# Performance work log

Hardware: AMD Instinct MI355X
Metric: run time of the kernel (lower is better)

## Reference

```python
import jax, jax.numpy as jnp
import numpy as np

N_NODES = 100000
N_EDGES = 1000000
D = 128           # operand size = 4 segments of u=32
N_SEG = 4


def setup_inputs() -> dict:
    key = jax.random.key(0)
    k1, k2, k3, k4, k5 = jax.random.split(key, 5)
    x = jax.random.normal(k1, (N_NODES, D), dtype=jnp.float32)   # node features (input 0)
    y = jax.random.normal(k2, (N_EDGES, D), dtype=jnp.float32)   # per-edge features (input 1)
    coeffs = jax.random.normal(k3, (N_SEG,), dtype=jnp.float32)  # stacked path coefficients, one per path (seg_i, seg_i, seg_i)
    src = jax.random.randint(k4, (N_EDGES,), 0, N_NODES, dtype=jnp.int64)  # input_indices[0]
    dst = jax.random.randint(k5, (N_EDGES,), 0, N_NODES, dtype=jnp.int64)  # output_indices[0]
    return {"x": x, "y": y, "coeffs": coeffs, "src": src, "dst": dst, "n_nodes": N_NODES}


def reference(x, y, coeffs, src, dst, n_nodes):
    # Segmented TP, subscripts 'u_u_u': per path p=(i,i,i), out_seg_i = c_i * x_seg_i * y_seg_i.
    # Broadcast per-segment path coefficient across its u=32 lanes.
    seg_size = x.shape[-1] // coeffs.shape[0]
    c = jnp.repeat(coeffs, seg_size)                 # [D]
    # gather (input_indices) -> fused elementwise TP -> scatter-add (output_indices)
    prod = x[src] * y * c                            # [E, D]
    out = jax.ops.segment_sum(prod, dst, num_segments=n_nodes)  # [N, D]
    return out
```

## Files before the change

### kernel.cpp

```cpp
#include <hip/hip_runtime.h>

#define N_EDGES  1000000
#define N_NODES  100000
#define DIM      128

#define WS_COUNTS   0
#define WS_COUNTS2  100000
#define WS_OFFSETS  200000
#define WS_BLKSUMS  300000
#define WS_BLKOFFS  300128
#define WS_SORTED   300256

#define SCAN_CHUNK  1024
#define NBLK        ((N_NODES + SCAN_CHUNK - 1) / SCAN_CHUNK)

__global__ void __launch_bounds__(256)
hist_kernel(const int* __restrict__ dst, unsigned* __restrict__ counts)
{
    int e = blockIdx.x * 256 + threadIdx.x;
    if (e < N_EDGES) atomicAdd(&counts[dst[e]], 1u);
}

__global__ void __launch_bounds__(256)
reduce_blocks(const unsigned* __restrict__ counts, unsigned* __restrict__ blkSums)
{
    __shared__ unsigned lds[256];
    int b = blockIdx.x, t = threadIdx.x;
    int base = b * SCAN_CHUNK + t * 4;
    unsigned s = 0;
    #pragma unroll
    for (int k = 0; k < 4; k++) { int i = base + k; if (i < N_NODES) s += counts[i]; }
    lds[t] = s; __syncthreads();
    for (int off = 128; off > 0; off >>= 1) {
        if (t < off) lds[t] += lds[t + off];
        __syncthreads();
    }
    if (t == 0) blkSums[b] = lds[0];
}

__global__ void scan_sums(const unsigned* __restrict__ blkSums, unsigned* __restrict__ blkOffs)
{
    if (threadIdx.x == 0) {
        unsigned r = 0;
        for (int i = 0; i < NBLK; i++) { blkOffs[i] = r; r += blkSums[i]; }
    }
}

__global__ void __launch_bounds__(256)
scan_blocks(const unsigned* __restrict__ counts, const unsigned* __restrict__ blkOffs,
            unsigned* __restrict__ offsets)
{
    __shared__ unsigned lds[256];
    int b = blockIdx.x, t = threadIdx.x;
    int base = b * SCAN_CHUNK + t * 4;
    unsigned v[4]; unsigned s = 0;
    #pragma unroll
    for (int k = 0; k < 4; k++) { int i = base + k; v[k] = (i < N_NODES) ? counts[i] : 0u; s += v[k]; }
    lds[t] = s; __syncthreads();
    for (int off = 1; off < 256; off <<= 1) {
        unsigned add = (t >= off) ? lds[t - off] : 0u;
        __syncthreads();
        lds[t] += add;
        __syncthreads();
    }
    unsigned excl = (t == 0) ? 0u : lds[t - 1];
    unsigned run = blkOffs[b] + excl;
    #pragma unroll
    for (int k = 0; k < 4; k++) { int i = base + k; if (i < N_NODES) offsets[i] = run; run += v[k]; }
}

__global__ void __launch_bounds__(256)
scatter_kernel(const int* __restrict__ dst, const unsigned* __restrict__ offsets,
               unsigned* __restrict__ cursors, unsigned* __restrict__ sorted)
{
    int e = blockIdx.x * 256 + threadIdx.x;
    if (e >= N_EDGES) return;
    int d = dst[e];
    unsigned pos = offsets[d] + atomicAdd(&cursors[d], 1u);
    sorted[pos] = (unsigned)e;
}

__global__ void __launch_bounds__(256)
gather_reduce(const float* __restrict__ x, const float* __restrict__ y,
              const float* __restrict__ coeffs, const int* __restrict__ src,
              const unsigned* __restrict__ offsets, const unsigned* __restrict__ counts,
              const unsigned* __restrict__ sorted, float* __restrict__ out)
{
    int wave = threadIdx.x >> 6;
    int lane = threadIdx.x & 63;
    int n = blockIdx.x * 4 + wave;
    if (n >= N_NODES) return;

    const int col = lane * 2;
    float c = coeffs[lane >> 4];
    unsigned start = offsets[n];
    unsigned cnt   = counts[n];
    unsigned j = start, end = start + cnt;

    float ax = 0.f, ay = 0.f;
    for (; j + 2 <= end; j += 2) {
        unsigned e0 = sorted[j], e1 = sorted[j + 1];
        int s0 = src[e0], s1 = src[e1];
        float2 y0 = *reinterpret_cast<const float2*>(y + (size_t)e0 * DIM + col);
        float2 x0 = *reinterpret_cast<const float2*>(x + (size_t)s0 * DIM + col);
        float2 y1 = *reinterpret_cast<const float2*>(y + (size_t)e1 * DIM + col);
        float2 x1 = *reinterpret_cast<const float2*>(x + (size_t)s1 * DIM + col);
        ax += x0.x * y0.x; ay += x0.y * y0.y;
        ax += x1.x * y1.x; ay += x1.y * y1.y;
    }
    if (j < end) {
        unsigned e0 = sorted[j];
        int s0 = src[e0];
        float2 y0 = *reinterpret_cast<const float2*>(y + (size_t)e0 * DIM + col);
        float2 x0 = *reinterpret_cast<const float2*>(x + (size_t)s0 * DIM + col);
        ax += x0.x * y0.x; ay += x0.y * y0.y;
    }
    float2 r; r.x = c * ax; r.y = c * ay;
    *reinterpret_cast<float2*>(out + (size_t)n * DIM + col) = r;
}

extern "C" void kernel_launch(void* const* d_in, const int* in_sizes, int n_in,
                              void* d_out, int out_size, void* d_ws, size_t ws_size,
                              hipStream_t stream)
{
    const float* x      = (const float*)d_in[0];
    const float* y      = (const float*)d_in[1];
    const float* coeffs = (const float*)d_in[2];
    const int*   src    = (const int*)d_in[3];
    const int*   dst    = (const int*)d_in[4];
    float* out = (float*)d_out;

    unsigned* ws = (unsigned*)d_ws;
    unsigned* counts  = ws + WS_COUNTS;
    unsigned* cursors = ws + WS_COUNTS2;
    unsigned* offsets = ws + WS_OFFSETS;
    unsigned* blkSums = ws + WS_BLKSUMS;
    unsigned* blkOffs = ws + WS_BLKOFFS;
    unsigned* sorted  = ws + WS_SORTED;

    hipMemsetAsync(d_ws, 0, 200000 * sizeof(unsigned), stream);

    hist_kernel<<<(N_EDGES + 255) / 256, 256, 0, stream>>>(dst, counts);
    reduce_blocks<<<NBLK, 256, 0, stream>>>(counts, blkSums);
    scan_sums<<<1, 64, 0, stream>>>(blkSums, blkOffs);
    scan_blocks<<<NBLK, 256, 0, stream>>>(counts, blkOffs, offsets);
    scatter_kernel<<<(N_EDGES + 255) / 256, 256, 0, stream>>>(dst, offsets, cursors, sorted);
    gather_reduce<<<(N_NODES + 3) / 4, 256, 0, stream>>>(x, y, coeffs, src, offsets, counts, sorted, out);
}
```

Before: 867.1 us.

## Replace prefix scan with atomic bucket allocation and pack src into sorted pairs

Replaces the three-kernel prefix scan with one kernel that gives each wave a contiguous bucket range through an atomic counter. Buckets are no longer globally ordered, but each node's range stays contiguous. The scatter now stores (edge, src) pairs, so the gather no longer does a dependent lookup into src. The gather splits each wave into two halves that handle alternate edges with float4 loads, nontemporal loads for y and nontemporal stores, then combines the halves with a cross-lane shuffle. The aim is to cut launch count and the latency of dependent gathers, at the cost of a larger pairs buffer.

```diff
diff --git a/kernel.cpp b/kernel.cpp
--- a/kernel.cpp
+++ b/kernel.cpp
@@ -4,15 +4,13 @@
 #define N_NODES  100000
 #define DIM      128
 
+typedef float f32x4 __attribute__((ext_vector_type(4)));
+
 #define WS_COUNTS   0
-#define WS_COUNTS2  100000
-#define WS_OFFSETS  200000
-#define WS_BLKSUMS  300000
-#define WS_BLKOFFS  300128
-#define WS_SORTED   300256
-
-#define SCAN_CHUNK  1024
-#define NBLK        ((N_NODES + SCAN_CHUNK - 1) / SCAN_CHUNK)
+#define WS_CURSORS  100000
+#define WS_CTR      200000
+#define WS_OFFSETS  200064
+#define WS_PAIRS    300064
 
 __global__ void __launch_bounds__(256)
 hist_kernel(const int* __restrict__ dst, unsigned* __restrict__ counts)
@@ -22,101 +20,98 @@
 }
 
 __global__ void __launch_bounds__(256)
-reduce_blocks(const unsigned* __restrict__ counts, unsigned* __restrict__ blkSums)
+alloc_offsets(const unsigned* __restrict__ counts, unsigned* __restrict__ offsets,
+              unsigned* __restrict__ ctr)
 {
-    __shared__ unsigned lds[256];
-    int b = blockIdx.x, t = threadIdx.x;
-    int base = b * SCAN_CHUNK + t * 4;
-    unsigned s = 0;
+    int n = blockIdx.x * 256 + threadIdx.x;
+    int lane = threadIdx.x & 63;
+    unsigned cnt = (n < N_NODES) ? counts[n] : 0u;
+
+    unsigned incl = cnt;
     #pragma unroll
-    for (int k = 0; k < 4; k++) { int i = base + k; if (i < N_NODES) s += counts[i]; }
-    lds[t] = s; __syncthreads();
-    for (int off = 128; off > 0; off >>= 1) {
-        if (t < off) lds[t] += lds[t + off];
-        __syncthreads();
+    for (int off = 1; off < 64; off <<= 1) {
+        unsigned v = __shfl_up(incl, off, 64);
+        if (lane >= off) incl += v;
     }
-    if (t == 0) blkSums[b] = lds[0];
-}
-
-__global__ void scan_sums(const unsigned* __restrict__ blkSums, unsigned* __restrict__ blkOffs)
-{
-    if (threadIdx.x == 0) {
-        unsigned r = 0;
-        for (int i = 0; i < NBLK; i++) { blkOffs[i] = r; r += blkSums[i]; }
-    }
+    unsigned total = __shfl(incl, 63, 64);
+    unsigned base = 0;
+    if (lane == 63) base = atomicAdd(ctr, total);
+    base = __shfl(base, 63, 64);
+    if (n < N_NODES) offsets[n] = base + incl - cnt;
 }
 
 __global__ void __launch_bounds__(256)
-scan_blocks(const unsigned* __restrict__ counts, const unsigned* __restrict__ blkOffs,
-            unsigned* __restrict__ offsets)
-{
-    __shared__ unsigned lds[256];
-    int b = blockIdx.x, t = threadIdx.x;
-    int base = b * SCAN_CHUNK + t * 4;
-    unsigned v[4]; unsigned s = 0;
-    #pragma unroll
-    for (int k = 0; k < 4; k++) { int i = base + k; v[k] = (i < N_NODES) ? counts[i] : 0u; s += v[k]; }
-    lds[t] = s; __syncthreads();
-    for (int off = 1; off < 256; off <<= 1) {
-        unsigned add = (t >= off) ? lds[t - off] : 0u;
-        __syncthreads();
-        lds[t] += add;
-        __syncthreads();
-    }
-    unsigned excl = (t == 0) ? 0u : lds[t - 1];
-    unsigned run = blkOffs[b] + excl;
-    #pragma unroll
-    for (int k = 0; k < 4; k++) { int i = base + k; if (i < N_NODES) offsets[i] = run; run += v[k]; }
-}
-
-__global__ void __launch_bounds__(256)
-scatter_kernel(const int* __restrict__ dst, const unsigned* __restrict__ offsets,
-               unsigned* __restrict__ cursors, unsigned* __restrict__ sorted)
+scatter_kernel(const int* __restrict__ dst, const int* __restrict__ src,
+               const unsigned* __restrict__ offsets, unsigned* __restrict__ cursors,
+               uint2* __restrict__ pairs)
 {
     int e = blockIdx.x * 256 + threadIdx.x;
     if (e >= N_EDGES) return;
     int d = dst[e];
     unsigned pos = offsets[d] + atomicAdd(&cursors[d], 1u);
-    sorted[pos] = (unsigned)e;
+    pairs[pos] = make_uint2((unsigned)e, (unsigned)src[e]);
+}
+
+__device__ __forceinline__ f32x4 ld_nt(const float* p)
+{
+    return __builtin_nontemporal_load(reinterpret_cast<const f32x4*>(p));
+}
+__device__ __forceinline__ f32x4 ld(const float* p)
+{
+    return *reinterpret_cast<const f32x4*>(p);
 }
 
 __global__ void __launch_bounds__(256)
 gather_reduce(const float* __restrict__ x, const float* __restrict__ y,
-              const float* __restrict__ coeffs, const int* __restrict__ src,
+              const float* __restrict__ coeffs,
               const unsigned* __restrict__ offsets, const unsigned* __restrict__ counts,
-              const unsigned* __restrict__ sorted, float* __restrict__ out)
+              const uint2* __restrict__ pairs, float* __restrict__ out)
 {
     int wave = threadIdx.x >> 6;
     int lane = threadIdx.x & 63;
     int n = blockIdx.x * 4 + wave;
     if (n >= N_NODES) return;
 
-    const int col = lane * 2;
-    float c = coeffs[lane >> 4];
+    int half = lane >> 5;
+    int l    = lane & 31;
+    int col  = l * 4;
+    float c  = coeffs[l >> 3];
+
     unsigned start = offsets[n];
     unsigned cnt   = counts[n];
-    unsigned j = start, end = start + cnt;
+    unsigned end   = start + cnt;
 
-    float ax = 0.f, ay = 0.f;
-    for (; j + 2 <= end; j += 2) {
-        unsigned e0 = sorted[j], e1 = sorted[j + 1];
-        int s0 = src[e0], s1 = src[e1];
-        float2 y0 = *reinterpret_cast<const float2*>(y + (size_t)e0 * DIM + col);
-        float2 x0 = *reinterpret_cast<const float2*>(x + (size_t)s0 * DIM + col);
-        float2 y1 = *reinterpret_cast<const float2*>(y + (size_t)e1 * DIM + col);
-        float2 x1 = *reinterpret_cast<const float2*>(x + (size_t)s1 * DIM + col);
-        ax += x0.x * y0.x; ay += x0.y * y0.y;
-        ax += x1.x * y1.x; ay += x1.y * y1.y;
+    float a0 = 0.f, a1 = 0.f, a2 = 0.f, a3 = 0.f;
+    float b0 = 0.f, b1 = 0.f, b2 = 0.f, b3 = 0.f;
+
+    unsigned j = start + half;
+    for (; j + 2 < end; j += 4) {
+        uint2 p0 = pairs[j];
+        uint2 p1 = pairs[j + 2];
+        f32x4 y0 = ld_nt(y + (size_t)p0.x * DIM + col);
+        f32x4 x0 = ld  (x + (size_t)p0.y * DIM + col);
+        f32x4 y1 = ld_nt(y + (size_t)p1.x * DIM + col);
+        f32x4 x1 = ld  (x + (size_t)p1.y * DIM + col);
+        a0 += x0.x * y0.x; a1 += x0.y * y0.y; a2 += x0.z * y0.z; a3 += x0.w * y0.w;
+        b0 += x1.x * y1.x; b1 += x1.y * y1.y; b2 += x1.z * y1.z; b3 += x1.w * y1.w;
     }
     if (j < end) {
-        unsigned e0 = sorted[j];
-        int s0 = src[e0];
-        float2 y0 = *reinterpret_cast<const float2*>(y + (size_t)e0 * DIM + col);
-        float2 x0 = *reinterpret_cast<const float2*>(x + (size_t)s0 * DIM + col);
-        ax += x0.x * y0.x; ay += x0.y * y0.y;
+        uint2 p0 = pairs[j];
+        f32x4 y0 = ld_nt(y + (size_t)p0.x * DIM + col);
+        f32x4 x0 = ld  (x + (size_t)p0.y * DIM + col);
+        a0 += x0.x * y0.x; a1 += x0.y * y0.y; a2 += x0.z * y0.z; a3 += x0.w * y0.w;
     }
-    float2 r; r.x = c * ax; r.y = c * ay;
-    *reinterpret_cast<float2*>(out + (size_t)n * DIM + col) = r;
+
+    a0 += b0; a1 += b1; a2 += b2; a3 += b3;
+    a0 += __shfl_xor(a0, 32, 64);
+    a1 += __shfl_xor(a1, 32, 64);
+    a2 += __shfl_xor(a2, 32, 64);
+    a3 += __shfl_xor(a3, 32, 64);
+
+    if (half == 0) {
+        f32x4 r = { c * a0, c * a1, c * a2, c * a3 };
+        __builtin_nontemporal_store(r, reinterpret_cast<f32x4*>(out + (size_t)n * DIM + col));
+    }
 }
 
 extern "C" void kernel_launch(void* const* d_in, const int* in_sizes, int n_in,
@@ -130,20 +125,17 @@
     const int*   dst    = (const int*)d_in[4];
     float* out = (float*)d_out;
 
-    unsigned* ws = (unsigned*)d_ws;
+    unsigned* ws      = (unsigned*)d_ws;
     unsigned* counts  = ws + WS_COUNTS;
-    unsigned* cursors = ws + WS_COUNTS2;
+    unsigned* cursors = ws + WS_CURSORS;
+    unsigned* ctr     = ws + WS_CTR;
     unsigned* offsets = ws + WS_OFFSETS;
-    unsigned* blkSums = ws + WS_BLKSUMS;
-    unsigned* blkOffs = ws + WS_BLKOFFS;
-    unsigned* sorted  = ws + WS_SORTED;
+    uint2*    pairs   = (uint2*)(ws + WS_PAIRS);
 
-    hipMemsetAsync(d_ws, 0, 200000 * sizeof(unsigned), stream);
+    hipMemsetAsync(d_ws, 0, WS_OFFSETS * sizeof(unsigned), stream);
 
-    hist_kernel<<<(N_EDGES + 255) / 256, 256, 0, stream>>>(dst, counts);
-    reduce_blocks<<<NBLK, 256, 0, stream>>>(counts, blkSums);
-    scan_sums<<<1, 64, 0, stream>>>(blkSums, blkOffs);
-    scan_blocks<<<NBLK, 256, 0, stream>>>(counts, blkOffs, offsets);
-    scatter_kernel<<<(N_EDGES + 255) / 256, 256, 0, stream>>>(dst, offsets, cursors, sorted);
-    gather_reduce<<<(N_NODES + 3) / 4, 256, 0, stream>>>(x, y, coeffs, src, offsets, counts, sorted, out);
+    hist_kernel   <<<(N_EDGES + 255) / 256, 256, 0, stream>>>(dst, counts);
+    alloc_offsets <<<(N_NODES + 255) / 256, 256, 0, stream>>>(counts, offsets, ctr);
+    scatter_kernel<<<(N_EDGES + 255) / 256, 256, 0, stream>>>(dst, src, offsets, cursors, pairs);
+    gather_reduce <<<(N_NODES + 3) / 4,     256, 0, stream>>>(x, y, coeffs, offsets, counts, pairs, out);
 }
```

Measured after the change: 824.7 us. 4.9% less time.
